# Kernel optimization log

Measured on AMD Instinct MI355X. Metric: run time of the kernel, lower is better.

The kernel has to match this reference:

```python
import jax, jax.numpy as jnp
import numpy as np

N_NODES = 100000
N_EDGES = 1600000
FEAT = 128
HID = 128
N_GRAPHS = 128


def setup_inputs() -> dict:
    key = jax.random.key(0)
    ks = jax.random.split(key, 20)
    inp = {
        'x': jax.random.normal(ks[0], (N_NODES, FEAT), dtype=jnp.float32),
        'edge_index': jax.random.randint(ks[1], (2, N_EDGES), 0, N_NODES, dtype=jnp.int32),
        'batch': jnp.sort(jax.random.randint(ks[2], (N_NODES,), 0, N_GRAPHS, dtype=jnp.int32)),
        'layer_K': 1,
    }
    # Xavier-uniform weights, zero biases (matches LinearPrune.reset_parameters)
    i = 3
    for l in range(3):
        in_dim = FEAT if l == 0 else HID
        lim1 = float(np.sqrt(6.0 / (in_dim + HID)))
        lim2 = float(np.sqrt(6.0 / (HID + HID)))
        inp[f'W1_l{l}'] = jax.random.uniform(ks[i], (HID, in_dim), jnp.float32, -lim1, lim1); i += 1
        inp[f'b1_l{l}'] = jnp.zeros((HID,), jnp.float32)
        inp[f'W2_l{l}'] = jax.random.uniform(ks[i], (HID, HID), jnp.float32, -lim2, lim2); i += 1
        inp[f'b2_l{l}'] = jnp.zeros((HID,), jnp.float32)
    return inp


def _gin_conv(x, src, dst, W1, b1, W2, b2, k):
    # GINConvPrune.forward with skip=1, eps=0, prune=False
    out = x
    for _ in range(k):  # k = layer_K, static int (deterministic finetune/eval path)
        # propagate: gather neighbor feats then scatter-add at dst nodes
        agg = jax.ops.segment_sum(out[src], dst, num_segments=x.shape[0])
        out = (out + agg) * 0.5
    if k == 0:
        out = jax.ops.segment_sum(x[src], dst, num_segments=x.shape[0])
    out = out + x  # (1 + eps) * x_r with eps = 0
    h = jax.nn.relu(out @ W1.T + b1)
    return h @ W2.T + b2


def reference(x, edge_index, batch, layer_K,
              W1_l0, b1_l0, W2_l0, b2_l0,
              W1_l1, b1_l1, W2_l1, b2_l1,
              W1_l2, b1_l2, W2_l2, b2_l2):
    src, dst = edge_index[0], edge_index[1]
    params = [(W1_l0, b1_l0, W2_l0, b2_l0),
              (W1_l1, b1_l1, W2_l1, b2_l1),
              (W1_l2, b1_l2, W2_l2, b2_l2)]
    k = int(layer_K)
    h = x
    pooled = []
    for (W1, b1, W2, b2) in params:
        h = _gin_conv(h, src, dst, W1, b1, W2, b2, k)
        h = jax.nn.relu(h)  # outer self.act
        pooled.append(jax.ops.segment_sum(h, batch, num_segments=N_GRAPHS))  # global_add_pool
    return jnp.concatenate(pooled, axis=1)  # [G, 3*HID]
```

## Files before the change

kernel.cpp:

```cpp
#include <hip/hip_runtime.h>

#define NN 100000
#define NE 1600000
#define FEAT 128
#define NGRAPH 128
#define BSHIFT 9
#define NB 196
#define NCHUNK 400
#define CHUNK 4000

typedef __attribute__((ext_vector_type(8))) short bf16x8;
typedef __attribute__((ext_vector_type(4))) float f32x4;

__device__ __forceinline__ unsigned short f2bf(float f) {
    unsigned u = __float_as_uint(f);
    return (unsigned short)((u + 0x7fffu + ((u >> 16) & 1u)) >> 16);
}
__device__ __forceinline__ float bf2f(unsigned short h) {
    return __uint_as_float(((unsigned)h) << 16);
}

__global__ __launch_bounds__(256)
void wsplit_frag_kernel(const float* __restrict__ W, short* __restrict__ Wf)
{
    int i = blockIdx.x * 256 + threadIdx.x;
    int o = i >> 7, k = i & 127;
    float f = W[i];
    unsigned short h = f2bf(f);
    short lo = (short)f2bf(f - bf2f(h));
    int ct = o >> 4, lr = o & 15, kc = k >> 5, q = (k >> 3) & 3, j = k & 7;
    int idx = (kc * 8 + ct) * 512 + ((q << 4) | lr) * 8 + j;
    Wf[idx] = (short)h;
    Wf[16384 + idx] = lo;
}

__global__ __launch_bounds__(256)
void p1a_count(const int* __restrict__ ei, int* __restrict__ cnt_T)
{
    __shared__ int hist[NB];
    const int b = blockIdx.x, tid = threadIdx.x;
    for (int i = tid; i < NB; i += 256) hist[i] = 0;
    __syncthreads();
    const int e0 = b * CHUNK;
    for (int e = e0 + tid; e < e0 + CHUNK; e += 256)
        atomicAdd(&hist[ei[NE + e] >> BSHIFT], 1);
    __syncthreads();
    for (int k = tid; k < NB; k += 256) cnt_T[k * NCHUNK + b] = hist[k];
}

__global__ __launch_bounds__(1024)
void scan1_kernel(const int* __restrict__ in, int* __restrict__ out,
                  int* __restrict__ bsum, int n)
{
    __shared__ int sh[1024];
    const int tid = threadIdx.x;
    const int gid = blockIdx.x * 1024 + tid;
    int v = (gid < n) ? in[gid] : 0;
    sh[tid] = v;
    __syncthreads();
    #pragma unroll
    for (int d = 1; d < 1024; d <<= 1) {
        int t = (tid >= d) ? sh[tid - d] : 0;
        __syncthreads();
        sh[tid] += t;
        __syncthreads();
    }
    if (gid < n) out[gid] = sh[tid] - v;
    if (tid == 1023) bsum[blockIdx.x] = sh[1023];
}

__global__ __launch_bounds__(128)
void scan2_kernel(int* __restrict__ bsum, int nb)
{
    __shared__ int sh[128];
    const int tid = threadIdx.x;
    int v = (tid < nb) ? bsum[tid] : 0;
    sh[tid] = v;
    __syncthreads();
    #pragma unroll
    for (int d = 1; d < 128; d <<= 1) {
        int t = (tid >= d) ? sh[tid - d] : 0;
        __syncthreads();
        sh[tid] += t;
        __syncthreads();
    }
    if (tid < nb) bsum[tid] = sh[tid] - v;
}

__global__ __launch_bounds__(1024)
void scan3g_kernel(int* __restrict__ arr, const int* __restrict__ bsum, int n)
{
    const int gid = blockIdx.x * 1024 + threadIdx.x;
    if (gid < n) arr[gid] += bsum[blockIdx.x];
}

__global__ __launch_bounds__(256)
void p1b_scatter(const int* __restrict__ ei, const int* __restrict__ offs_T,
                 int2* __restrict__ ebuf)
{
    __shared__ int cur[NB];
    const int b = blockIdx.x, tid = threadIdx.x;
    for (int i = tid; i < NB; i += 256) cur[i] = offs_T[i * NCHUNK + b];
    __syncthreads();
    const int e0 = b * CHUNK;
    for (int e = e0 + tid; e < e0 + CHUNK; e += 256) {
        int s = ei[e], d = ei[NE + e];
        int pos = atomicAdd(&cur[d >> BSHIFT], 1);
        ebuf[pos] = make_int2(s, d);
    }
}

__global__ __launch_bounds__(512)
void p2_csr(const int2* __restrict__ ebuf, const int* __restrict__ offs_T,
            int* __restrict__ off, int* __restrict__ csr)
{
    __shared__ int degc[512];
    __shared__ int sh[512];
    const int k = blockIdx.x, tid = threadIdx.x;
    const int base = k << BSHIFT;
    const int bs = offs_T[k * NCHUNK];
    const int be = (k == NB - 1) ? NE : offs_T[(k + 1) * NCHUNK];
    degc[tid] = 0;
    __syncthreads();
    for (int e = bs + tid; e < be; e += 512)
        atomicAdd(&degc[ebuf[e].y - base], 1);
    __syncthreads();
    int v = degc[tid];
    sh[tid] = v;
    __syncthreads();
    #pragma unroll
    for (int d = 1; d < 512; d <<= 1) {
        int t = (tid >= d) ? sh[tid - d] : 0;
        __syncthreads();
        sh[tid] += t;
        __syncthreads();
    }
    const int excl = bs + sh[tid] - v;
    const int n = base + tid;
    if (n <= NN) off[n] = excl;
    degc[tid] = excl;
    __syncthreads();
    for (int e = bs + tid; e < be; e += 512) {
        int2 p = ebuf[e];
        int slot = atomicAdd(&degc[p.y - base], 1);
        csr[slot] = p.x;
    }
}

__global__ __launch_bounds__(256)
void aggregate_split_kernel(const float* __restrict__ h, const int* __restrict__ off,
                            const int* __restrict__ csr, short* __restrict__ xH,
                            short* __restrict__ xL, int nn)
{
    const int node = blockIdx.x * 4 + (threadIdx.x >> 6);
    if (node >= nn) return;
    const int lane = threadIdx.x & 63;
    const int s = off[node], e = off[node + 1];
    float2 acc = make_float2(0.f, 0.f);
    for (int base = s; base < e; base += 64) {
        const int cnt = min(64, e - base);
        int src_l = (base + lane < e) ? csr[base + lane] : 0;
        for (int jb = 0; jb < cnt; jb += 16) {
            float2 v[16];
            #pragma unroll
            for (int q = 0; q < 16; ++q) {
                int sq = __shfl(src_l, (jb + q) & 63);
                v[q] = reinterpret_cast<const float2*>(h + (size_t)sq * FEAT)[lane];
            }
            #pragma unroll
            for (int q = 0; q < 16; ++q) {
                if (jb + q < cnt) { acc.x += v[q].x; acc.y += v[q].y; }
            }
        }
    }
    float2 hv = reinterpret_cast<const float2*>(h + (size_t)node * FEAT)[lane];
    float ox = (hv.x + acc.x) * 0.5f + hv.x;
    float oy = (hv.y + acc.y) * 0.5f + hv.y;
    unsigned short hx = f2bf(ox), hy = f2bf(oy);
    short2 hi2 = make_short2((short)hx, (short)hy);
    short2 lo2 = make_short2((short)f2bf(ox - bf2f(hx)), (short)f2bf(oy - bf2f(hy)));
    reinterpret_cast<short2*>(xH + (size_t)node * FEAT)[lane] = hi2;
    reinterpret_cast<short2*>(xL + (size_t)node * FEAT)[lane] = lo2;
}

__global__ __launch_bounds__(512)
void gemm_mfma3_kernel(const short* __restrict__ aH, const short* __restrict__ aL,
                       const short* __restrict__ Wf, const float* __restrict__ bias,
                       float* __restrict__ outF, short* __restrict__ outH,
                       short* __restrict__ outL, int n_nodes)
{
    __shared__ short wlds[32768];
    const int tid = threadIdx.x;
    const int lane = tid & 63;
    const int w = tid >> 6;
    const int lr = lane & 15;
    const int lk = (lane >> 4) << 3;
    const int row0 = blockIdx.x * 256 + w * 32;

    {
        const bf16x8* src = reinterpret_cast<const bf16x8*>(Wf);
        bf16x8* dst = reinterpret_cast<bf16x8*>(wlds);
        #pragma unroll
        for (int it = 0; it < 8; ++it)
            dst[it * 512 + tid] = src[it * 512 + tid];
    }

    const int r0 = row0 + lr;
    const int r1 = row0 + 16 + lr;
    const size_t rb0 = (size_t)r0 * FEAT + lk;
    const size_t rb1 = (size_t)r1 * FEAT + lk;
    const bool v0 = (r0 < n_nodes), v1 = (r1 < n_nodes);
    bf16x8 z = {};
    bf16x8 ah[4][2], al[4][2];
    #pragma unroll
    for (int kc = 0; kc < 4; ++kc) {
        ah[kc][0] = v0 ? *reinterpret_cast<const bf16x8*>(&aH[rb0 + kc * 32]) : z;
        al[kc][0] = v0 ? *reinterpret_cast<const bf16x8*>(&aL[rb0 + kc * 32]) : z;
        ah[kc][1] = v1 ? *reinterpret_cast<const bf16x8*>(&aH[rb1 + kc * 32]) : z;
        al[kc][1] = v1 ? *reinterpret_cast<const bf16x8*>(&aL[rb1 + kc * 32]) : z;
    }
    __syncthreads();

    f32x4 acc[2][8] = {};
    #pragma unroll
    for (int kc = 0; kc < 4; ++kc) {
        #pragma unroll
        for (int ct = 0; ct < 8; ++ct) {
            const int ra = (kc * 8 + ct) * 512 + lane * 8;
            bf16x8 bh = *reinterpret_cast<const bf16x8*>(&wlds[ra]);
            bf16x8 bl = *reinterpret_cast<const bf16x8*>(&wlds[16384 + ra]);
            #pragma unroll
            for (int rt = 0; rt < 2; ++rt) {
                acc[rt][ct] = __builtin_amdgcn_mfma_f32_16x16x32_bf16(ah[kc][rt], bh, acc[rt][ct], 0, 0, 0);
                acc[rt][ct] = __builtin_amdgcn_mfma_f32_16x16x32_bf16(al[kc][rt], bh, acc[rt][ct], 0, 0, 0);
                acc[rt][ct] = __builtin_amdgcn_mfma_f32_16x16x32_bf16(ah[kc][rt], bl, acc[rt][ct], 0, 0, 0);
            }
        }
    }

    #pragma unroll
    for (int rt = 0; rt < 2; ++rt) {
        const int rbase = row0 + rt * 16 + ((lane >> 4) << 2);
        #pragma unroll
        for (int ct = 0; ct < 8; ++ct) {
            const int col = ct * 16 + lr;
            const float b = bias[col];
            #pragma unroll
            for (int j = 0; j < 4; ++j) {
                const int n = rbase + j;
                if (n < n_nodes) {
                    float v = fmaxf(acc[rt][ct][j] + b, 0.f);
                    if (outF) {
                        outF[(size_t)n * FEAT + col] = v;
                    } else {
                        unsigned short hh = f2bf(v);
                        outH[(size_t)n * FEAT + col] = (short)hh;
                        outL[(size_t)n * FEAT + col] = (short)f2bf(v - bf2f(hh));
                    }
                }
            }
        }
    }
}

__global__ __launch_bounds__(512)
void pool_kernel(const float* __restrict__ y, const int* __restrict__ batch,
                 float* __restrict__ out, int n_nodes, int layer)
{
    const int g = blockIdx.x;
    int lo = 0, hi = n_nodes;
    while (lo < hi) { int mid = (lo + hi) >> 1; if (batch[mid] < g) lo = mid + 1; else hi = mid; }
    const int start = lo;
    hi = n_nodes;
    while (lo < hi) { int mid = (lo + hi) >> 1; if (batch[mid] < g + 1) lo = mid + 1; else hi = mid; }
    const int end = lo;

    const int tid = threadIdx.x;
    const int f = tid & 127;
    const int q = tid >> 7;
    float sum = 0.f;
    for (int n = start + q; n < end; n += 4)
        sum += y[(size_t)n * FEAT + f];

    __shared__ float red[512];
    red[tid] = sum;
    __syncthreads();
    if (tid < 128)
        out[g * (3 * FEAT) + layer * FEAT + tid]
            = red[tid] + red[tid + 128] + red[tid + 256] + red[tid + 384];
}

__global__ __launch_bounds__(256)
void scatter_kernel(const float* __restrict__ h, const int* __restrict__ ei,
                    float* __restrict__ agg, int n_edges)
{
    int e = blockIdx.x * 4 + (threadIdx.x >> 6);
    if (e >= n_edges) return;
    int lane = threadIdx.x & 63;
    int s = ei[e];
    int d = ei[n_edges + e];
    float2 v = reinterpret_cast<const float2*>(h + (size_t)s * FEAT)[lane];
    float* ap = agg + (size_t)d * FEAT + lane * 2;
    atomicAdd(ap, v.x);
    atomicAdd(ap + 1, v.y);
}

__global__ __launch_bounds__(256)
void combine_kernel(const float* __restrict__ h, float* __restrict__ agg_xeff, size_t n4)
{
    size_t i = (size_t)blockIdx.x * 256 + threadIdx.x;
    if (i >= n4) return;
    float4 a = reinterpret_cast<const float4*>(h)[i];
    float4 g = reinterpret_cast<float4*>(agg_xeff)[i];
    float4 o;
    o.x = (a.x + g.x) * 0.5f + a.x;
    o.y = (a.y + g.y) * 0.5f + a.y;
    o.z = (a.z + g.z) * 0.5f + a.z;
    o.w = (a.w + g.w) * 0.5f + a.w;
    reinterpret_cast<float4*>(agg_xeff)[i] = o;
}

__global__ __launch_bounds__(256, 2)
void gemm_relu_kernel(const float* __restrict__ A, const float* __restrict__ W,
                      const float* __restrict__ bias, float* __restrict__ out, int n_nodes)
{
    __shared__ float xt[64][128];
    __shared__ float wt[64][128];
    const int tid = threadIdx.x;
    const int row0 = blockIdx.x * 128;
    const int r  = tid >> 1;
    const int ks = (tid & 1) << 5;
    const int tn = (tid >> 4) << 3;
    const int to = (tid & 15) << 3;
    float acc[8][8] = {};

    for (int c = 0; c < 2; ++c) {
        const int k0 = c * 64;
        {
            const float4* wrow = reinterpret_cast<const float4*>(W + r * FEAT + k0 + ks);
            #pragma unroll
            for (int i = 0; i < 8; ++i) {
                float4 w4 = wrow[i];
                int kk = ks + i * 4;
                wt[kk + 0][r] = w4.x; wt[kk + 1][r] = w4.y;
                wt[kk + 2][r] = w4.z; wt[kk + 3][r] = w4.w;
            }
        }
        {
            const int n = row0 + r;
            if (n < n_nodes) {
                const float4* ar = reinterpret_cast<const float4*>(A + (size_t)n * FEAT + k0 + ks);
                #pragma unroll
                for (int i = 0; i < 8; ++i) {
                    float4 a4 = ar[i];
                    int kk = ks + i * 4;
                    xt[kk + 0][r] = a4.x; xt[kk + 1][r] = a4.y;
                    xt[kk + 2][r] = a4.z; xt[kk + 3][r] = a4.w;
                }
            } else {
                #pragma unroll
                for (int i = 0; i < 8; ++i) {
                    int kk = ks + i * 4;
                    xt[kk + 0][r] = 0.f; xt[kk + 1][r] = 0.f;
                    xt[kk + 2][r] = 0.f; xt[kk + 3][r] = 0.f;
                }
            }
        }
        __syncthreads();
        #pragma unroll 4
        for (int k = 0; k < 64; ++k) {
            float4 x0 = *reinterpret_cast<const float4*>(&xt[k][tn]);
            float4 x1 = *reinterpret_cast<const float4*>(&xt[k][tn + 4]);
            float4 w0 = *reinterpret_cast<const float4*>(&wt[k][to]);
            float4 w1 = *reinterpret_cast<const float4*>(&wt[k][to + 4]);
            float xv[8] = {x0.x, x0.y, x0.z, x0.w, x1.x, x1.y, x1.z, x1.w};
            float wv[8] = {w0.x, w0.y, w0.z, w0.w, w1.x, w1.y, w1.z, w1.w};
            #pragma unroll
            for (int i = 0; i < 8; ++i)
                #pragma unroll
                for (int j = 0; j < 8; ++j)
                    acc[i][j] = fmaf(xv[i], wv[j], acc[i][j]);
        }
        __syncthreads();
    }

    float bv[8];
    #pragma unroll
    for (int j = 0; j < 8; ++j) bv[j] = bias[to + j];
    #pragma unroll
    for (int i = 0; i < 8; ++i) {
        int n = row0 + tn + i;
        if (n >= n_nodes) break;
        float4 o0, o1;
        o0.x = fmaxf(acc[i][0] + bv[0], 0.f);
        o0.y = fmaxf(acc[i][1] + bv[1], 0.f);
        o0.z = fmaxf(acc[i][2] + bv[2], 0.f);
        o0.w = fmaxf(acc[i][3] + bv[3], 0.f);
        o1.x = fmaxf(acc[i][4] + bv[4], 0.f);
        o1.y = fmaxf(acc[i][5] + bv[5], 0.f);
        o1.z = fmaxf(acc[i][6] + bv[6], 0.f);
        o1.w = fmaxf(acc[i][7] + bv[7], 0.f);
        float* op = out + (size_t)n * FEAT + to;
        *reinterpret_cast<float4*>(op) = o0;
        *reinterpret_cast<float4*>(op + 4) = o1;
    }
}

extern "C" void kernel_launch(void* const* d_in, const int* in_sizes, int n_in,
                              void* d_out, int out_size, void* d_ws, size_t ws_size,
                              hipStream_t stream)
{
    const float* x     = (const float*)d_in[0];
    const int*   ei    = (const int*)d_in[1];
    const int*   batch = (const int*)d_in[2];
    const float* W1[3] = {(const float*)d_in[4], (const float*)d_in[8],  (const float*)d_in[12]};
    const float* b1[3] = {(const float*)d_in[5], (const float*)d_in[9],  (const float*)d_in[13]};
    const float* W2[3] = {(const float*)d_in[6], (const float*)d_in[10], (const float*)d_in[14]};
    const float* b2[3] = {(const float*)d_in[7], (const float*)d_in[11], (const float*)d_in[15]};

    const size_t nf = (size_t)NN * FEAT;
    float* outp = (float*)d_out;
    const int gemm_grid = (NN + 255) / 256;
    const int M = NB * NCHUNK;
    const int scanM_blocks = (M + 1023) / 1024;
    const int WN = FEAT * FEAT;

    const size_t need_full = 3 * nf * 4 + (size_t)(NN + 1 + NE) * 4 + (size_t)12 * WN * 2;

    if (ws_size >= need_full) {
        short* xeffH = (short*)d_ws;
        short* xeffL = xeffH + nf;
        short* h1H   = xeffL + nf;
        short* h1L   = h1H + nf;
        float* bufC  = (float*)(h1L + nf);
        int* off     = (int*)(bufC + nf);
        int* csr     = off + (NN + 1);
        short* wbase = (short*)(csr + NE);
        short* wf[6];
        for (int i = 0; i < 6; ++i) wf[i] = wbase + (size_t)i * 2 * WN;
        int* cnt_T  = (int*)xeffH;
        int* offs_T = cnt_T + M;
        int* bsum   = offs_T + M;
        int2* ebuf  = (int2*)h1H;

        const float* Ws[6] = {W1[0], W2[0], W1[1], W2[1], W1[2], W2[2]};
        for (int i = 0; i < 6; ++i)
            wsplit_frag_kernel<<<WN / 256, 256, 0, stream>>>(Ws[i], wf[i]);

        p1a_count<<<NCHUNK, 256, 0, stream>>>(ei, cnt_T);
        scan1_kernel<<<scanM_blocks, 1024, 0, stream>>>(cnt_T, offs_T, bsum, M);
        scan2_kernel<<<1, 128, 0, stream>>>(bsum, scanM_blocks);
        scan3g_kernel<<<scanM_blocks, 1024, 0, stream>>>(offs_T, bsum, M);
        p1b_scatter<<<NCHUNK, 256, 0, stream>>>(ei, offs_T, ebuf);
        p2_csr<<<NB, 512, 0, stream>>>(ebuf, offs_T, off, csr);

        const float* h = x;
        for (int l = 0; l < 3; ++l) {
            aggregate_split_kernel<<<(NN + 3) / 4, 256, 0, stream>>>(h, off, csr, xeffH, xeffL, NN);
            gemm_mfma3_kernel<<<gemm_grid, 512, 0, stream>>>(xeffH, xeffL, wf[2 * l],
                                                             b1[l], nullptr, h1H, h1L, NN);
            gemm_mfma3_kernel<<<gemm_grid, 512, 0, stream>>>(h1H, h1L, wf[2 * l + 1],
                                                             b2[l], bufC, nullptr, nullptr, NN);
            pool_kernel<<<NGRAPH, 512, 0, stream>>>(bufC, batch, outp, NN, l);
            h = bufC;
        }
    } else if (ws_size >= 3 * nf * 4) {
        float* bufA = (float*)d_ws;
        float* bufB = bufA + nf;
        float* bufC = bufB + nf;
        const int gg = (NN + 127) / 128;
        const float* h = x;
        for (int l = 0; l < 3; ++l) {
            hipMemsetAsync(bufA, 0, nf * 4, stream);
            scatter_kernel<<<(NE + 3) / 4, 256, 0, stream>>>(h, ei, bufA, NE);
            combine_kernel<<<(int)((nf / 4 + 255) / 256), 256, 0, stream>>>(h, bufA, nf / 4);
            gemm_relu_kernel<<<gg, 256, 0, stream>>>(bufA, W1[l], b1[l], bufB, NN);
            gemm_relu_kernel<<<gg, 256, 0, stream>>>(bufB, W2[l], b2[l], bufC, NN);
            pool_kernel<<<NGRAPH, 512, 0, stream>>>(bufC, batch, outp, NN, l);
            h = bufC;
        }
    }
}
```

Before: 786.6 us.

## Interleave hi/lo bf16 split activations and swap MFMA operands for vector epilogue

Stores each split activation as one packed 32-bit word (hi and lo bf16 halves) instead of two separate arrays, so the GEMM loads one contiguous stream per row. The GEMM swaps its MFMA operands so each lane owns four consecutive output columns, which allows float4 and uint4 epilogue stores instead of scalar ones. It also prefetches the next K-chunk of activations while the current one computes, and sets a launch-bounds occupancy hint. Unpacking the interleaved halves adds some ALU work, and the more complex prefetch adds register pressure.

```diff
diff --git a/kernel.cpp b/kernel.cpp
--- a/kernel.cpp
+++ b/kernel.cpp
@@ -11,6 +11,9 @@
 
 typedef __attribute__((ext_vector_type(8))) short bf16x8;
 typedef __attribute__((ext_vector_type(4))) float f32x4;
+typedef __attribute__((ext_vector_type(4))) unsigned u32x4;
+
+union U4 { u32x4 u; bf16x8 v; };
 
 __device__ __forceinline__ unsigned short f2bf(float f) {
     unsigned u = __float_as_uint(f);
@@ -18,6 +21,17 @@
 }
 __device__ __forceinline__ float bf2f(unsigned short h) {
     return __uint_as_float(((unsigned)h) << 16);
+}
+__device__ __forceinline__ uint2 unpack2(unsigned p0, unsigned p1) {
+    return make_uint2((p0 & 0xffffu) | (p1 << 16), (p0 >> 16) | (p1 & 0xffff0000u));
+}
+__device__ __forceinline__ void unpack8(u32x4 a, u32x4 b, bf16x8& hv, bf16x8& lv) {
+    uint2 r0 = unpack2(a.x, a.y), r1 = unpack2(a.z, a.w);
+    uint2 r2 = unpack2(b.x, b.y), r3 = unpack2(b.z, b.w);
+    U4 h, l;
+    h.u = (u32x4){r0.x, r1.x, r2.x, r3.x};
+    l.u = (u32x4){r0.y, r1.y, r2.y, r3.y};
+    hv = h.v; lv = l.v;
 }
 
 __global__ __launch_bounds__(256)
@@ -148,9 +162,8 @@
 }
 
 __global__ __launch_bounds__(256)
-void aggregate_split_kernel(const float* __restrict__ h, const int* __restrict__ off,
-                            const int* __restrict__ csr, short* __restrict__ xH,
-                            short* __restrict__ xL, int nn)
+void aggregate_pack_kernel(const float* __restrict__ h, const int* __restrict__ off,
+                           const int* __restrict__ csr, unsigned* __restrict__ xP, int nn)
 {
     const int node = blockIdx.x * 4 + (threadIdx.x >> 6);
     if (node >= nn) return;
@@ -177,24 +190,23 @@
     float ox = (hv.x + acc.x) * 0.5f + hv.x;
     float oy = (hv.y + acc.y) * 0.5f + hv.y;
     unsigned short hx = f2bf(ox), hy = f2bf(oy);
-    short2 hi2 = make_short2((short)hx, (short)hy);
-    short2 lo2 = make_short2((short)f2bf(ox - bf2f(hx)), (short)f2bf(oy - bf2f(hy)));
-    reinterpret_cast<short2*>(xH + (size_t)node * FEAT)[lane] = hi2;
-    reinterpret_cast<short2*>(xL + (size_t)node * FEAT)[lane] = lo2;
-}
-
-__global__ __launch_bounds__(512)
-void gemm_mfma3_kernel(const short* __restrict__ aH, const short* __restrict__ aL,
-                       const short* __restrict__ Wf, const float* __restrict__ bias,
-                       float* __restrict__ outF, short* __restrict__ outH,
-                       short* __restrict__ outL, int n_nodes)
+    unsigned wx = (unsigned)hx | ((unsigned)f2bf(ox - bf2f(hx)) << 16);
+    unsigned wy = (unsigned)hy | ((unsigned)f2bf(oy - bf2f(hy)) << 16);
+    uint2 pw = make_uint2(wx, wy);
+    *reinterpret_cast<uint2*>(&xP[(size_t)node * FEAT + lane * 2]) = pw;
+}
+
+__global__ __launch_bounds__(512, 4)
+void gemm_mfma5_kernel(const unsigned* __restrict__ aP, const short* __restrict__ Wf,
+                       const float* __restrict__ bias, float* __restrict__ outF,
+                       unsigned* __restrict__ outP, int n_nodes)
 {
     __shared__ short wlds[32768];
     const int tid = threadIdx.x;
     const int lane = tid & 63;
     const int w = tid >> 6;
     const int lr = lane & 15;
-    const int lk = (lane >> 4) << 3;
+    const int lq = lane >> 4;
     const int row0 = blockIdx.x * 256 + w * 32;
 
     {
@@ -205,59 +217,76 @@
             dst[it * 512 + tid] = src[it * 512 + tid];
     }
 
-    const int r0 = row0 + lr;
-    const int r1 = row0 + 16 + lr;
-    const size_t rb0 = (size_t)r0 * FEAT + lk;
-    const size_t rb1 = (size_t)r1 * FEAT + lk;
-    const bool v0 = (r0 < n_nodes), v1 = (r1 < n_nodes);
-    bf16x8 z = {};
-    bf16x8 ah[4][2], al[4][2];
+    const int n0 = row0 + lr;
+    const int n1 = row0 + 16 + lr;
+    const bool v0 = (n0 < n_nodes), v1 = (n1 < n_nodes);
+    const size_t rb0 = (size_t)n0 * FEAT + lq * 8;
+    const size_t rb1 = (size_t)n1 * FEAT + lq * 8;
+    u32x4 zz = {};
+
+    u32x4 pa0a = v0 ? *reinterpret_cast<const u32x4*>(&aP[rb0])     : zz;
+    u32x4 pa0b = v0 ? *reinterpret_cast<const u32x4*>(&aP[rb0 + 4]) : zz;
+    u32x4 pa1a = v1 ? *reinterpret_cast<const u32x4*>(&aP[rb1])     : zz;
+    u32x4 pa1b = v1 ? *reinterpret_cast<const u32x4*>(&aP[rb1 + 4]) : zz;
+    __syncthreads();
+
+    f32x4 acc[2][8] = {};
+    bf16x8 ah0, al0, ah1, al1;
+    unpack8(pa0a, pa0b, ah0, al0);
+    unpack8(pa1a, pa1b, ah1, al1);
+
     #pragma unroll
     for (int kc = 0; kc < 4; ++kc) {
-        ah[kc][0] = v0 ? *reinterpret_cast<const bf16x8*>(&aH[rb0 + kc * 32]) : z;
-        al[kc][0] = v0 ? *reinterpret_cast<const bf16x8*>(&aL[rb0 + kc * 32]) : z;
-        ah[kc][1] = v1 ? *reinterpret_cast<const bf16x8*>(&aH[rb1 + kc * 32]) : z;
-        al[kc][1] = v1 ? *reinterpret_cast<const bf16x8*>(&aL[rb1 + kc * 32]) : z;
-    }
-    __syncthreads();
-
-    f32x4 acc[2][8] = {};
-    #pragma unroll
-    for (int kc = 0; kc < 4; ++kc) {
+        u32x4 n0a = zz, n0b = zz, n1a = zz, n1b = zz;
+        if (kc < 3) {
+            const int ko = (kc + 1) * 32;
+            n0a = v0 ? *reinterpret_cast<const u32x4*>(&aP[rb0 + ko])     : zz;
+            n0b = v0 ? *reinterpret_cast<const u32x4*>(&aP[rb0 + ko + 4]) : zz;
+            n1a = v1 ? *reinterpret_cast<const u32x4*>(&aP[rb1 + ko])     : zz;
+            n1b = v1 ? *reinterpret_cast<const u32x4*>(&aP[rb1 + ko + 4]) : zz;
+        }
         #pragma unroll
         for (int ct = 0; ct < 8; ++ct) {
             const int ra = (kc * 8 + ct) * 512 + lane * 8;
             bf16x8 bh = *reinterpret_cast<const bf16x8*>(&wlds[ra]);
             bf16x8 bl = *reinterpret_cast<const bf16x8*>(&wlds[16384 + ra]);
-            #pragma unroll
-            for (int rt = 0; rt < 2; ++rt) {
-                acc[rt][ct] = __builtin_amdgcn_mfma_f32_16x16x32_bf16(ah[kc][rt], bh, acc[rt][ct], 0, 0, 0);
-                acc[rt][ct] = __builtin_amdgcn_mfma_f32_16x16x32_bf16(al[kc][rt], bh, acc[rt][ct], 0, 0, 0);
-                acc[rt][ct] = __builtin_amdgcn_mfma_f32_16x16x32_bf16(ah[kc][rt], bl, acc[rt][ct], 0, 0, 0);
-            }
-        }
-    }
-
-    #pragma unroll
-    for (int rt = 0; rt < 2; ++rt) {
-        const int rbase = row0 + rt * 16 + ((lane >> 4) << 2);
+            acc[0][ct] = __builtin_amdgcn_mfma_f32_16x16x32_bf16(bh, ah0, acc[0][ct], 0, 0, 0);
+            acc[0][ct] = __builtin_amdgcn_mfma_f32_16x16x32_bf16(bh, al0, acc[0][ct], 0, 0, 0);
+            acc[0][ct] = __builtin_amdgcn_mfma_f32_16x16x32_bf16(bl, ah0, acc[0][ct], 0, 0, 0);
+            acc[1][ct] = __builtin_amdgcn_mfma_f32_16x16x32_bf16(bh, ah1, acc[1][ct], 0, 0, 0);
+            acc[1][ct] = __builtin_amdgcn_mfma_f32_16x16x32_bf16(bh, al1, acc[1][ct], 0, 0, 0);
+            acc[1][ct] = __builtin_amdgcn_mfma_f32_16x16x32_bf16(bl, ah1, acc[1][ct], 0, 0, 0);
+        }
+        if (kc < 3) {
+            unpack8(n0a, n0b, ah0, al0);
+            unpack8(n1a, n1b, ah1, al1);
+        }
+    }
+
+    #pragma unroll
+    for (int nt = 0; nt < 2; ++nt) {
+        const int n = row0 + nt * 16 + lr;
+        if (n >= n_nodes) continue;
         #pragma unroll
         for (int ct = 0; ct < 8; ++ct) {
-            const int col = ct * 16 + lr;
-            const float b = bias[col];
-            #pragma unroll
-            for (int j = 0; j < 4; ++j) {
-                const int n = rbase + j;
-                if (n < n_nodes) {
-                    float v = fmaxf(acc[rt][ct][j] + b, 0.f);
-                    if (outF) {
-                        outF[(size_t)n * FEAT + col] = v;
-                    } else {
-                        unsigned short hh = f2bf(v);
-                        outH[(size_t)n * FEAT + col] = (short)hh;
-                        outL[(size_t)n * FEAT + col] = (short)f2bf(v - bf2f(hh));
-                    }
-                }
+            const int c0 = ct * 16 + lq * 4;
+            float4 bv = *reinterpret_cast<const float4*>(&bias[c0]);
+            f32x4 a = acc[nt][ct];
+            float e0 = fmaxf(a[0] + bv.x, 0.f);
+            float e1 = fmaxf(a[1] + bv.y, 0.f);
+            float e2 = fmaxf(a[2] + bv.z, 0.f);
+            float e3 = fmaxf(a[3] + bv.w, 0.f);
+            if (outF) {
+                float4 o = make_float4(e0, e1, e2, e3);
+                *reinterpret_cast<float4*>(&outF[(size_t)n * FEAT + c0]) = o;
+            } else {
+                unsigned short h0 = f2bf(e0), h1 = f2bf(e1), h2 = f2bf(e2), h3 = f2bf(e3);
+                u32x4 pw;
+                pw.x = (unsigned)h0 | ((unsigned)f2bf(e0 - bf2f(h0)) << 16);
+                pw.y = (unsigned)h1 | ((unsigned)f2bf(e1 - bf2f(h1)) << 16);
+                pw.z = (unsigned)h2 | ((unsigned)f2bf(e2 - bf2f(h2)) << 16);
+                pw.w = (unsigned)h3 | ((unsigned)f2bf(e3 - bf2f(h3)) << 16);
+                *reinterpret_cast<u32x4*>(&outP[(size_t)n * FEAT + c0]) = pw;
             }
         }
     }
@@ -428,20 +457,18 @@
     const size_t need_full = 3 * nf * 4 + (size_t)(NN + 1 + NE) * 4 + (size_t)12 * WN * 2;
 
     if (ws_size >= need_full) {
-        short* xeffH = (short*)d_ws;
-        short* xeffL = xeffH + nf;
-        short* h1H   = xeffL + nf;
-        short* h1L   = h1H + nf;
-        float* bufC  = (float*)(h1L + nf);
-        int* off     = (int*)(bufC + nf);
-        int* csr     = off + (NN + 1);
-        short* wbase = (short*)(csr + NE);
+        unsigned* xeffP = (unsigned*)d_ws;
+        unsigned* h1P   = xeffP + nf;
+        float* bufC     = (float*)(h1P + nf);
+        int* off        = (int*)(bufC + nf);
+        int* csr        = off + (NN + 1);
+        short* wbase    = (short*)(csr + NE);
         short* wf[6];
         for (int i = 0; i < 6; ++i) wf[i] = wbase + (size_t)i * 2 * WN;
-        int* cnt_T  = (int*)xeffH;
+        int* cnt_T  = (int*)xeffP;
         int* offs_T = cnt_T + M;
         int* bsum   = offs_T + M;
-        int2* ebuf  = (int2*)h1H;
+        int2* ebuf  = (int2*)h1P;
 
         const float* Ws[6] = {W1[0], W2[0], W1[1], W2[1], W1[2], W2[2]};
         for (int i = 0; i < 6; ++i)
@@ -456,11 +483,11 @@
 
         const float* h = x;
         for (int l = 0; l < 3; ++l) {
-            aggregate_split_kernel<<<(NN + 3) / 4, 256, 0, stream>>>(h, off, csr, xeffH, xeffL, NN);
-            gemm_mfma3_kernel<<<gemm_grid, 512, 0, stream>>>(xeffH, xeffL, wf[2 * l],
-                                                             b1[l], nullptr, h1H, h1L, NN);
-            gemm_mfma3_kernel<<<gemm_grid, 512, 0, stream>>>(h1H, h1L, wf[2 * l + 1],
-                                                             b2[l], bufC, nullptr, nullptr, NN);
+            aggregate_pack_kernel<<<(NN + 3) / 4, 256, 0, stream>>>(h, off, csr, xeffP, NN);
+            gemm_mfma5_kernel<<<gemm_grid, 512, 0, stream>>>(xeffP, wf[2 * l], b1[l],
+                                                             nullptr, h1P, NN);
+            gemm_mfma5_kernel<<<gemm_grid, 512, 0, stream>>>(h1P, wf[2 * l + 1], b2[l],
+                                                             bufC, nullptr, NN);
             pool_kernel<<<NGRAPH, 512, 0, stream>>>(bufC, batch, outp, NN, l);
             h = bufC;
         }
```

Result: faster. 721.8 us (-8.2%).
